# Kernel tuning notes

Hardware: AMD Instinct MI355X
Metric: run time of the kernel (lower is better)

Reference implementation:

```python
import jax, jax.numpy as jnp
import numpy as np

B = 1_000_000
NG = 4          # distance_embed_dim -> 4x0e scalars per edge feature
MAX_OFF = 5.0   # max_cross_offset (GaussianSmearing stop)

# e3nn FullyConnectedTensorProduct path coefficients:
#   coeff = sqrt(dim(ir_out) / fan_in_elements) * w3j_entry
# where w3j entries are 1 (000), 1/sqrt(3) (011/101/110), eps/sqrt(6) (111).
# tp1: irreps (4x0e+1e) x (4x0e+1e) -> 20x0e + 5x1e
#   fan_in(0e) = 4*4 + 1*1 = 17 ; fan_in(1e) = 4*1 + 1*4 + 1*1 = 9
C1_000 = (1.0 / 17.0) ** 0.5
C1_110 = (1.0 / 17.0) ** 0.5 / 3.0 ** 0.5
C1_011 = (3.0 / 9.0) ** 0.5 / 3.0 ** 0.5
C1_101 = C1_011
C1_111 = (3.0 / 9.0) ** 0.5 / 6.0 ** 0.5
# tp2: (20x0e+5x1e) x (4x0e+1e) -> 9x0e + 1x1e
#   fan_in(0e) = 20*4 + 5*1 = 85 ; fan_in(1e) = 20*1 + 5*4 + 5*1 = 45
C2_000 = (1.0 / 85.0) ** 0.5
C2_110 = (1.0 / 85.0) ** 0.5 / 3.0 ** 0.5
C2_011 = (3.0 / 45.0) ** 0.5 / 3.0 ** 0.5
C2_101 = C2_011
C2_111 = (3.0 / 45.0) ** 0.5 / 6.0 ** 0.5


def setup_inputs() -> dict:
    key = jax.random.key(0)
    ks = jax.random.split(key, 12)
    f32 = jnp.float32
    return dict(
        ligand=jax.random.normal(ks[0], (B, 4, 3), f32),
        receptor=jax.random.normal(ks[1], (B, 4, 3), f32) + 1.0,
        # tp1 weights (mul-1 axes squeezed): paths 000,110,011,101,111
        w1_000=jax.random.normal(ks[2], (NG, NG, 20), f32),
        w1_110=jax.random.normal(ks[3], (20,), f32),
        w1_011=jax.random.normal(ks[4], (NG, 5), f32),
        w1_101=jax.random.normal(ks[5], (NG, 5), f32),
        w1_111=jax.random.normal(ks[6], (5,), f32),
        # tp2 weights
        w2_000=jax.random.normal(ks[7], (20, NG, 9), f32),
        w2_110=jax.random.normal(ks[8], (5, 9), f32),
        w2_011=jax.random.normal(ks[9], (20,), f32),
        w2_101=jax.random.normal(ks[10], (5, NG), f32),
        w2_111=jax.random.normal(ks[11], (5,), f32),
    )


def _forward(ligand, receptor, w1_000, w1_110, w1_011, w1_101, w1_111,
             w2_000, w2_110, w2_011, w2_101, w2_111):
    edge_vec = ligand - receptor                                 # (B,4,3)
    dist = jnp.sqrt(jnp.sum(edge_vec * edge_vec, -1, keepdims=True))  # (B,4,1)
    offset = jnp.linspace(0.0, MAX_OFF, NG).astype(ligand.dtype)  # (NG,)
    coeff = -0.5 / (offset[1] - offset[0]) ** 2
    emb = jnp.exp(coeff * (dist - offset) ** 2)                  # (B,4,NG)
    unit = edge_vec / dist                                       # (B,4,3)
    s1, v1 = emb[:, 1], unit[:, 1]
    s2, v2 = emb[:, 2], unit[:, 2]
    s3, v3 = emb[:, 3], unit[:, 3]
    # ---- tp1: (s1,v1) x (s2,v2) -> S (B,20), V (B,5,3) ----
    dot12 = jnp.sum(v1 * v2, -1)                                 # (B,)
    S = (C1_000 * jnp.einsum('uvw,bu,bv->bw', w1_000, s1, s2)
         + C1_110 * dot12[:, None] * w1_110)
    cr12 = jnp.cross(v1, v2)                                     # (B,3)
    V = (C1_011 * jnp.einsum('uw,bu,bk->bwk', w1_011, s1, v2)
         + C1_101 * jnp.einsum('vw,bv,bk->bwk', w1_101, s2, v1)
         + C1_111 * w1_111[None, :, None] * cr12[:, None, :])
    # ---- tp2: (S,V) x (s3,v3) -> out (B,12) = 9x0e + 1x1e ----
    Vd3 = jnp.einsum('buk,bk->bu', V, v3)                        # (B,5)
    S2 = (C2_000 * jnp.einsum('uvw,bu,bv->bw', w2_000, S, s3)
          + C2_110 * jnp.einsum('uw,bu->bw', w2_110, Vd3))
    Vx3 = jnp.cross(V, v3[:, None, :])                           # (B,5,3)
    V2 = (C2_011 * jnp.einsum('u,bu,bk->bk', w2_011, S, v3)
          + C2_101 * jnp.einsum('uv,buk,bv->bk', w2_101, V, s3)
          + C2_111 * jnp.einsum('u,buk->bk', w2_111, Vx3))
    return jnp.concatenate([S2, V2], -1)                         # (B,12)


def reference(ligand, receptor, w1_000, w1_110, w1_011, w1_101, w1_111,
              w2_000, w2_110, w2_011, w2_101, w2_111):
    out = _forward(ligand, receptor, w1_000, w1_110, w1_011, w1_101, w1_111,
                   w2_000, w2_110, w2_011, w2_101, w2_111)
    s_rot, s_tr = out[:, :3], out[:, 3:6]
    t_rot, t_tr = out[:, 6:9], out[:, 9:12]
    return s_rot, s_tr, t_rot, t_tr
```

## Files before the change

kernel.cpp:

```cpp
#include <hip/hip_runtime.h>
#include <math.h>


#define K_A   (0.10846522890932808f * 0.24253562503633297f)
#define K_B   (0.10846522890932808f * 0.14002800840979312f)
#define K_P   (0.06262242910851495f * 0.33333333333333333f)
#define K_Q   (0.06262242910851495f * 0.33333333333333333f)
#define K_R   (0.06262242910851495f * 0.23570226039551584f)
#define K_WB  (0.14907119849998599f * 0.24253562503633297f)
#define K_CB  (0.14907119849998599f * 0.14002800840979312f)
#define K_WA  (0.14907119849998599f * 0.33333333333333333f)
#define K_WBT (0.14907119849998599f * 0.33333333333333333f)
#define K_WC  (0.14907119849998599f * 0.23570226039551584f)
#define K_WA3 (0.10540925533894598f * 0.33333333333333333f)
#define K_WB3 (0.10540925533894598f * 0.33333333333333333f)
#define K_WC3 (0.10540925533894598f * 0.23570226039551584f)

#define EX_WB   720
#define EX_CB   736
#define EX_WA   740
#define EX_WBT  756
#define EX_WC   772
#define EX_WA3  776
#define EX_WB3  780
#define EX_WC3  784
#define N_WS    785

__global__ void fd8_prep(const float* __restrict__ w1_000, const float* __restrict__ w1_110,
                         const float* __restrict__ w1_011, const float* __restrict__ w1_101,
                         const float* __restrict__ w1_111, const float* __restrict__ w2_000,
                         const float* __restrict__ w2_110, const float* __restrict__ w2_011,
                         const float* __restrict__ w2_101, const float* __restrict__ w2_111,
                         float* __restrict__ ws)
{
    int j = threadIdx.x;
    if (j >= N_WS) return;
    float val = 0.f;
    if (j < 720) {
        int r = j / 9, c = j - r * 9;
        if (r < 64) {
            int pq = r >> 2, v = r & 3;
            float a = 0.f;
            for (int u = 0; u < 20; ++u)
                a = fmaf(w1_000[pq * 20 + u], w2_000[u * 36 + v * 9 + c], a);
            val = K_A * a;
        } else if (r < 68) {
            int v = r - 64; float a = 0.f;
            for (int u = 0; u < 20; ++u)
                a = fmaf(w1_110[u], w2_000[u * 36 + v * 9 + c], a);
            val = K_B * a;
        } else if (r < 72) {
            int u = r - 68; float a = 0.f;
            for (int m = 0; m < 5; ++m)
                a = fmaf(w1_011[u * 5 + m], w2_110[m * 9 + c], a);
            val = K_P * a;
        } else if (r < 76) {
            int u = r - 72; float a = 0.f;
            for (int m = 0; m < 5; ++m)
                a = fmaf(w1_101[u * 5 + m], w2_110[m * 9 + c], a);
            val = K_Q * a;
        } else if (r == 76) {
            float a = 0.f;
            for (int m = 0; m < 5; ++m)
                a = fmaf(w1_111[m], w2_110[m * 9 + c], a);
            val = K_R * a;
        }
    } else {
        int k = j - 720;
        if (k < 16) {
            float a = 0.f;
            for (int u = 0; u < 20; ++u)
                a = fmaf(w2_011[u], w1_000[k * 20 + u], a);
            val = K_WB * a;
        } else if (k == 16) {
            float a = 0.f;
            for (int u = 0; u < 20; ++u)
                a = fmaf(w2_011[u], w1_110[u], a);
            val = K_CB * a;
        } else if (k >= 20 && k < 36) {
            int u = (k - 20) >> 2, v = (k - 20) & 3;
            float a = 0.f;
            for (int m = 0; m < 5; ++m)
                a = fmaf(w1_011[u * 5 + m], w2_101[m * 4 + v], a);
            val = K_WA * a;
        } else if (k >= 36 && k < 52) {
            int u = (k - 36) >> 2, v = (k - 36) & 3;
            float a = 0.f;
            for (int m = 0; m < 5; ++m)
                a = fmaf(w1_101[u * 5 + m], w2_101[m * 4 + v], a);
            val = K_WBT * a;
        } else if (k >= 52 && k < 56) {
            int v = k - 52; float a = 0.f;
            for (int m = 0; m < 5; ++m)
                a = fmaf(w1_111[m], w2_101[m * 4 + v], a);
            val = K_WC * a;
        } else if (k >= 56 && k < 60) {
            int u = k - 56; float a = 0.f;
            for (int m = 0; m < 5; ++m)
                a = fmaf(w2_111[m], w1_011[u * 5 + m], a);
            val = K_WA3 * a;
        } else if (k >= 60 && k < 64) {
            int v = k - 60; float a = 0.f;
            for (int m = 0; m < 5; ++m)
                a = fmaf(w2_111[m], w1_101[v * 5 + m], a);
            val = K_WB3 * a;
        } else if (k == 64) {
            float a = 0.f;
            for (int m = 0; m < 5; ++m)
                a = fmaf(w2_111[m], w1_111[m], a);
            val = K_WC3 * a;
        }
    }
    ws[j] = val;
}

__global__ __launch_bounds__(256) void
fd8(const float* __restrict__ lig, const float* __restrict__ rec,
    const float* __restrict__ ws, float* __restrict__ out, int n)
{
    const int tid = blockIdx.x * 256 + threadIdx.x;
    if (tid >= n) return;

    const float4* L = (const float4*)(lig + (size_t)tid * 12);
    const float4* R = (const float4*)(rec + (size_t)tid * 12);
    float4 l0 = L[0], l1 = L[1], l2 = L[2];
    float4 r0 = R[0], r1 = R[1], r2 = R[2];

    float e1x = l0.w - r0.w, e1y = l1.x - r1.x, e1z = l1.y - r1.y;
    float e2x = l1.z - r1.z, e2y = l1.w - r1.w, e2z = l2.x - r2.x;
    float e3x = l2.y - r2.y, e3y = l2.z - r2.z, e3z = l2.w - r2.w;

    float n1 = fmaf(e1x, e1x, fmaf(e1y, e1y, e1z * e1z));
    float n2 = fmaf(e2x, e2x, fmaf(e2y, e2y, e2z * e2z));
    float n3sq = fmaf(e3x, e3x, fmaf(e3y, e3y, e3z * e3z));
    float i1 = __builtin_amdgcn_rsqf(n1);
    float i2 = __builtin_amdgcn_rsqf(n2);
    float i3 = __builtin_amdgcn_rsqf(n3sq);
    float d1 = n1 * i1, d2 = n2 * i2, d3 = n3sq * i3;

    float v1x = e1x * i1, v1y = e1y * i1, v1z = e1z * i1;
    float v2x = e2x * i2, v2y = e2y * i2, v2z = e2z * i2;
    float v3x = e3x * i3, v3y = e3y * i3, v3z = e3z * i3;

    const float coeff = -0.18f;
    const float o1 = 1.6666666f, o2 = 3.3333333f, o3 = 5.f;
    float s1[4], s2[4], s3[4];
    float x;
    x = d1;      s1[0] = __expf(coeff * x * x);
    x = d1 - o1; s1[1] = __expf(coeff * x * x);
    x = d1 - o2; s1[2] = __expf(coeff * x * x);
    x = d1 - o3; s1[3] = __expf(coeff * x * x);
    x = d2;      s2[0] = __expf(coeff * x * x);
    x = d2 - o1; s2[1] = __expf(coeff * x * x);
    x = d2 - o2; s2[2] = __expf(coeff * x * x);
    x = d2 - o3; s2[3] = __expf(coeff * x * x);
    x = d3;      s3[0] = __expf(coeff * x * x);
    x = d3 - o1; s3[1] = __expf(coeff * x * x);
    x = d3 - o2; s3[2] = __expf(coeff * x * x);
    x = d3 - o3; s3[3] = __expf(coeff * x * x);

    float dot12 = v1x * v2x + v1y * v2y + v1z * v2z;
    float d13   = v1x * v3x + v1y * v3y + v1z * v3z;
    float d23   = v2x * v3x + v2y * v3y + v2z * v3z;
    float c12x = v1y * v2z - v1z * v2y;
    float c12y = v1z * v2x - v1x * v2z;
    float c12z = v1x * v2y - v1y * v2x;
    float dtp  = c12x * v3x + c12y * v3y + c12z * v3z;

    float acc0 = 0.f, acc1 = 0.f, acc2 = 0.f, acc3 = 0.f, acc4 = 0.f;
    float acc5 = 0.f, acc6 = 0.f, acc7 = 0.f, acc8 = 0.f;

#define GROUP4(g, x0v, x1v, x2v, x3v) do { \
    const float* wp_ = ws + 36 * (g); \
    const float x0_ = (x0v), x1_ = (x1v), x2_ = (x2v), x3_ = (x3v); \
    acc0 = fmaf(x0_, wp_[0], acc0);  acc1 = fmaf(x0_, wp_[1], acc1); \
    acc2 = fmaf(x0_, wp_[2], acc2);  acc3 = fmaf(x0_, wp_[3], acc3); \
    acc4 = fmaf(x0_, wp_[4], acc4);  acc5 = fmaf(x0_, wp_[5], acc5); \
    acc6 = fmaf(x0_, wp_[6], acc6);  acc7 = fmaf(x0_, wp_[7], acc7); \
    acc8 = fmaf(x0_, wp_[8], acc8); \
    acc0 = fmaf(x1_, wp_[9], acc0);  acc1 = fmaf(x1_, wp_[10], acc1); \
    acc2 = fmaf(x1_, wp_[11], acc2); acc3 = fmaf(x1_, wp_[12], acc3); \
    acc4 = fmaf(x1_, wp_[13], acc4); acc5 = fmaf(x1_, wp_[14], acc5); \
    acc6 = fmaf(x1_, wp_[15], acc6); acc7 = fmaf(x1_, wp_[16], acc7); \
    acc8 = fmaf(x1_, wp_[17], acc8); \
    acc0 = fmaf(x2_, wp_[18], acc0); acc1 = fmaf(x2_, wp_[19], acc1); \
    acc2 = fmaf(x2_, wp_[20], acc2); acc3 = fmaf(x2_, wp_[21], acc3); \
    acc4 = fmaf(x2_, wp_[22], acc4); acc5 = fmaf(x2_, wp_[23], acc5); \
    acc6 = fmaf(x2_, wp_[24], acc6); acc7 = fmaf(x2_, wp_[25], acc7); \
    acc8 = fmaf(x2_, wp_[26], acc8); \
    acc0 = fmaf(x3_, wp_[27], acc0); acc1 = fmaf(x3_, wp_[28], acc1); \
    acc2 = fmaf(x3_, wp_[29], acc2); acc3 = fmaf(x3_, wp_[30], acc3); \
    acc4 = fmaf(x3_, wp_[31], acc4); acc5 = fmaf(x3_, wp_[32], acc5); \
    acc6 = fmaf(x3_, wp_[33], acc6); acc7 = fmaf(x3_, wp_[34], acc7); \
    acc8 = fmaf(x3_, wp_[35], acc8); \
} while (0)

    float sg = dot12 * ws[EX_CB];

#pragma unroll
    for (int p = 0; p < 4; ++p) {
#pragma unroll
        for (int q = 0; q < 4; ++q) {
            const int pq = p * 4 + q;
            float o = s1[p] * s2[q];
            sg = fmaf(o, ws[EX_WB + pq], sg);
            GROUP4(pq, o * s3[0], o * s3[1], o * s3[2], o * s3[3]);
        }
    }
    GROUP4(16, dot12 * s3[0], dot12 * s3[1], dot12 * s3[2], dot12 * s3[3]);
    GROUP4(17, d23 * s1[0], d23 * s1[1], d23 * s1[2], d23 * s1[3]);
    GROUP4(18, d13 * s2[0], d13 * s2[1], d13 * s2[2], d13 * s2[3]);
    {
        const float* wp = ws + 36 * 19;
        acc0 = fmaf(dtp, wp[0], acc0); acc1 = fmaf(dtp, wp[1], acc1);
        acc2 = fmaf(dtp, wp[2], acc2); acc3 = fmaf(dtp, wp[3], acc3);
        acc4 = fmaf(dtp, wp[4], acc4); acc5 = fmaf(dtp, wp[5], acc5);
        acc6 = fmaf(dtp, wp[6], acc6); acc7 = fmaf(dtp, wp[7], acc7);
        acc8 = fmaf(dtp, wp[8], acc8);
    }
#undef GROUP4

    float ta = 0.f, tb = 0.f;
#pragma unroll
    for (int u = 0; u < 4; ++u) {
        float da = fmaf(ws[EX_WA + u * 4 + 0], s3[0], fmaf(ws[EX_WA + u * 4 + 1], s3[1],
                   fmaf(ws[EX_WA + u * 4 + 2], s3[2], ws[EX_WA + u * 4 + 3] * s3[3])));
        float db = fmaf(ws[EX_WBT + u * 4 + 0], s3[0], fmaf(ws[EX_WBT + u * 4 + 1], s3[1],
                   fmaf(ws[EX_WBT + u * 4 + 2], s3[2], ws[EX_WBT + u * 4 + 3] * s3[3])));
        ta = fmaf(s1[u], da, ta);
        tb = fmaf(s2[u], db, tb);
    }
    float tc = fmaf(ws[EX_WC + 0], s3[0], fmaf(ws[EX_WC + 1], s3[1],
               fmaf(ws[EX_WC + 2], s3[2], ws[EX_WC + 3] * s3[3])));
    float wa = fmaf(ws[EX_WA3 + 0], s1[0], fmaf(ws[EX_WA3 + 1], s1[1],
               fmaf(ws[EX_WA3 + 2], s1[2], ws[EX_WA3 + 3] * s1[3])));
    float wb = fmaf(ws[EX_WB3 + 0], s2[0], fmaf(ws[EX_WB3 + 1], s2[1],
               fmaf(ws[EX_WB3 + 2], s2[2], ws[EX_WB3 + 3] * s2[3])));
    float wc = ws[EX_WC3];

    float c23x = v2y * v3z - v2z * v3y;
    float c23y = v2z * v3x - v2x * v3z;
    float c23z = v2x * v3y - v2y * v3x;
    float c13x = v1y * v3z - v1z * v3y;
    float c13y = v1z * v3x - v1x * v3z;
    float c13z = v1x * v3y - v1y * v3x;
    float ccrx = c12y * v3z - c12z * v3y;
    float ccry = c12z * v3x - c12x * v3z;
    float ccrz = c12x * v3y - c12y * v3x;

    float V2x = sg * v3x + ta * v2x + tb * v1x + tc * c12x + wa * c23x + wb * c13x + wc * ccrx;
    float V2y = sg * v3y + ta * v2y + tb * v1y + tc * c12y + wa * c23y + wb * c13y + wc * ccry;
    float V2z = sg * v3z + ta * v2z + tb * v1z + tc * c12z + wa * c23z + wb * c13z + wc * ccrz;

    const size_t n3 = (size_t)n * 3;
    const size_t base = (size_t)tid * 3;
    out[base + 0] = acc0;
    out[base + 1] = acc1;
    out[base + 2] = acc2;
    out[n3 + base + 0] = acc3;
    out[n3 + base + 1] = acc4;
    out[n3 + base + 2] = acc5;
    out[2 * n3 + base + 0] = acc6;
    out[2 * n3 + base + 1] = acc7;
    out[2 * n3 + base + 2] = acc8;
    out[3 * n3 + base + 0] = V2x;
    out[3 * n3 + base + 1] = V2y;
    out[3 * n3 + base + 2] = V2z;
}

extern "C" void kernel_launch(void* const* d_in, const int* in_sizes, int n_in,
                              void* d_out, int out_size, void* d_ws, size_t ws_size,
                              hipStream_t stream) {
    const float* lig = (const float*)d_in[0];
    const float* rec = (const float*)d_in[1];
    float* ws = (float*)d_ws;

    fd8_prep<<<1, 1024, 0, stream>>>(
        (const float*)d_in[2], (const float*)d_in[3], (const float*)d_in[4],
        (const float*)d_in[5], (const float*)d_in[6], (const float*)d_in[7],
        (const float*)d_in[8], (const float*)d_in[9], (const float*)d_in[10],
        (const float*)d_in[11], ws);

    int n = in_sizes[0] / 12;
    int blocks = (n + 255) / 256;
    fd8<<<blocks, 256, 0, stream>>>(lig, rec, ws, (float*)d_out, n);
}
```

Baseline: 162.6 us.

## Process two items per thread with packed FP32 FMAs and paired stores

Each thread now handles two batch items, computing geometry for both and then accumulating the 9 scalar outputs with two-wide vector FMAs (v2f) over a reordered weight layout, so one weight load pair serves two packed lanes. The prep kernel permutes the fused weight table into interleaved column pairs to match, and runs on four blocks. Output writes become float2 stores covering both items. The aim is to use packed FP32 math and halve the scalar weight loads per item, at the cost of more registers per thread and possibly lower occupancy.

```diff
diff --git a/kernel.cpp b/kernel.cpp
--- a/kernel.cpp
+++ b/kernel.cpp
@@ -26,40 +26,46 @@
 #define EX_WC3  784
 #define N_WS    785
 
-__global__ void fd8_prep(const float* __restrict__ w1_000, const float* __restrict__ w1_110,
-                         const float* __restrict__ w1_011, const float* __restrict__ w1_101,
-                         const float* __restrict__ w1_111, const float* __restrict__ w2_000,
-                         const float* __restrict__ w2_110, const float* __restrict__ w2_011,
-                         const float* __restrict__ w2_101, const float* __restrict__ w2_111,
-                         float* __restrict__ ws)
+typedef float v2f __attribute__((ext_vector_type(2)));
+
+__global__ void fd10_prep(const float* __restrict__ w1_000, const float* __restrict__ w1_110,
+                          const float* __restrict__ w1_011, const float* __restrict__ w1_101,
+                          const float* __restrict__ w1_111, const float* __restrict__ w2_000,
+                          const float* __restrict__ w2_110, const float* __restrict__ w2_011,
+                          const float* __restrict__ w2_101, const float* __restrict__ w2_111,
+                          float* __restrict__ ws)
 {
-    int j = threadIdx.x;
+    int j = blockIdx.x * 256 + threadIdx.x;
     if (j >= N_WS) return;
     float val = 0.f;
     if (j < 720) {
-        int r = j / 9, c = j - r * 9;
-        if (r < 64) {
-            int pq = r >> 2, v = r & 3;
+        int g = j / 36, slot = j - g * 36;
+        int r, c;
+        if (slot < 32) { r = (slot & 7) >> 1; c = ((slot >> 3) << 1) + (slot & 1); }
+        else           { r = slot - 32;       c = 8; }
+        int R = 4 * g + r;
+        if (R < 64) {
+            int pq = R >> 2, v = R & 3;
             float a = 0.f;
             for (int u = 0; u < 20; ++u)
                 a = fmaf(w1_000[pq * 20 + u], w2_000[u * 36 + v * 9 + c], a);
             val = K_A * a;
-        } else if (r < 68) {
-            int v = r - 64; float a = 0.f;
+        } else if (R < 68) {
+            int v = R - 64; float a = 0.f;
             for (int u = 0; u < 20; ++u)
                 a = fmaf(w1_110[u], w2_000[u * 36 + v * 9 + c], a);
             val = K_B * a;
-        } else if (r < 72) {
-            int u = r - 68; float a = 0.f;
+        } else if (R < 72) {
+            int u = R - 68; float a = 0.f;
             for (int m = 0; m < 5; ++m)
                 a = fmaf(w1_011[u * 5 + m], w2_110[m * 9 + c], a);
             val = K_P * a;
-        } else if (r < 76) {
-            int u = r - 72; float a = 0.f;
+        } else if (R < 76) {
+            int u = R - 72; float a = 0.f;
             for (int m = 0; m < 5; ++m)
                 a = fmaf(w1_101[u * 5 + m], w2_110[m * 9 + c], a);
             val = K_Q * a;
-        } else if (r == 76) {
+        } else if (R == 76) {
             float a = 0.f;
             for (int m = 0; m < 5; ++m)
                 a = fmaf(w1_111[m], w2_110[m * 9 + c], a);
@@ -114,158 +120,205 @@
     ws[j] = val;
 }
 
-__global__ __launch_bounds__(256) void
-fd8(const float* __restrict__ lig, const float* __restrict__ rec,
-    const float* __restrict__ ws, float* __restrict__ out, int n)
+struct ItemState {
+    float s1[4], s2[4], s3[4];
+    float dot12, d13, d23, dtp;
+    float v3x, v3y, v3z;
+    float px, py, pz;
+};
+
+__device__ __forceinline__ ItemState geom(const float4 l0, const float4 l1, const float4 l2,
+                                          const float4 r0, const float4 r1, const float4 r2,
+                                          const float* __restrict__ ws)
 {
-    const int tid = blockIdx.x * 256 + threadIdx.x;
-    if (tid >= n) return;
-
-    const float4* L = (const float4*)(lig + (size_t)tid * 12);
-    const float4* R = (const float4*)(rec + (size_t)tid * 12);
-    float4 l0 = L[0], l1 = L[1], l2 = L[2];
-    float4 r0 = R[0], r1 = R[1], r2 = R[2];
-
+    ItemState st;
     float e1x = l0.w - r0.w, e1y = l1.x - r1.x, e1z = l1.y - r1.y;
     float e2x = l1.z - r1.z, e2y = l1.w - r1.w, e2z = l2.x - r2.x;
     float e3x = l2.y - r2.y, e3y = l2.z - r2.z, e3z = l2.w - r2.w;
 
     float n1 = fmaf(e1x, e1x, fmaf(e1y, e1y, e1z * e1z));
     float n2 = fmaf(e2x, e2x, fmaf(e2y, e2y, e2z * e2z));
-    float n3sq = fmaf(e3x, e3x, fmaf(e3y, e3y, e3z * e3z));
+    float n3q = fmaf(e3x, e3x, fmaf(e3y, e3y, e3z * e3z));
     float i1 = __builtin_amdgcn_rsqf(n1);
     float i2 = __builtin_amdgcn_rsqf(n2);
-    float i3 = __builtin_amdgcn_rsqf(n3sq);
-    float d1 = n1 * i1, d2 = n2 * i2, d3 = n3sq * i3;
+    float i3 = __builtin_amdgcn_rsqf(n3q);
+    float d1 = n1 * i1, d2 = n2 * i2, d3 = n3q * i3;
 
     float v1x = e1x * i1, v1y = e1y * i1, v1z = e1z * i1;
     float v2x = e2x * i2, v2y = e2y * i2, v2z = e2z * i2;
-    float v3x = e3x * i3, v3y = e3y * i3, v3z = e3z * i3;
+    st.v3x = e3x * i3; st.v3y = e3y * i3; st.v3z = e3z * i3;
 
     const float coeff = -0.18f;
     const float o1 = 1.6666666f, o2 = 3.3333333f, o3 = 5.f;
-    float s1[4], s2[4], s3[4];
     float x;
-    x = d1;      s1[0] = __expf(coeff * x * x);
-    x = d1 - o1; s1[1] = __expf(coeff * x * x);
-    x = d1 - o2; s1[2] = __expf(coeff * x * x);
-    x = d1 - o3; s1[3] = __expf(coeff * x * x);
-    x = d2;      s2[0] = __expf(coeff * x * x);
-    x = d2 - o1; s2[1] = __expf(coeff * x * x);
-    x = d2 - o2; s2[2] = __expf(coeff * x * x);
-    x = d2 - o3; s2[3] = __expf(coeff * x * x);
-    x = d3;      s3[0] = __expf(coeff * x * x);
-    x = d3 - o1; s3[1] = __expf(coeff * x * x);
-    x = d3 - o2; s3[2] = __expf(coeff * x * x);
-    x = d3 - o3; s3[3] = __expf(coeff * x * x);
-
-    float dot12 = v1x * v2x + v1y * v2y + v1z * v2z;
-    float d13   = v1x * v3x + v1y * v3y + v1z * v3z;
-    float d23   = v2x * v3x + v2y * v3y + v2z * v3z;
+    x = d1;      st.s1[0] = __expf(coeff * x * x);
+    x = d1 - o1; st.s1[1] = __expf(coeff * x * x);
+    x = d1 - o2; st.s1[2] = __expf(coeff * x * x);
+    x = d1 - o3; st.s1[3] = __expf(coeff * x * x);
+    x = d2;      st.s2[0] = __expf(coeff * x * x);
+    x = d2 - o1; st.s2[1] = __expf(coeff * x * x);
+    x = d2 - o2; st.s2[2] = __expf(coeff * x * x);
+    x = d2 - o3; st.s2[3] = __expf(coeff * x * x);
+    x = d3;      st.s3[0] = __expf(coeff * x * x);
+    x = d3 - o1; st.s3[1] = __expf(coeff * x * x);
+    x = d3 - o2; st.s3[2] = __expf(coeff * x * x);
+    x = d3 - o3; st.s3[3] = __expf(coeff * x * x);
+
+    st.dot12 = v1x * v2x + v1y * v2y + v1z * v2z;
+    st.d13   = v1x * st.v3x + v1y * st.v3y + v1z * st.v3z;
+    st.d23   = v2x * st.v3x + v2y * st.v3y + v2z * st.v3z;
     float c12x = v1y * v2z - v1z * v2y;
     float c12y = v1z * v2x - v1x * v2z;
     float c12z = v1x * v2y - v1y * v2x;
-    float dtp  = c12x * v3x + c12y * v3y + c12z * v3z;
-
-    float acc0 = 0.f, acc1 = 0.f, acc2 = 0.f, acc3 = 0.f, acc4 = 0.f;
-    float acc5 = 0.f, acc6 = 0.f, acc7 = 0.f, acc8 = 0.f;
-
-#define GROUP4(g, x0v, x1v, x2v, x3v) do { \
+    st.dtp = c12x * st.v3x + c12y * st.v3y + c12z * st.v3z;
+
+    float ta = 0.f, tb = 0.f;
+#pragma unroll
+    for (int u = 0; u < 4; ++u) {
+        float da = fmaf(ws[EX_WA + u * 4 + 0], st.s3[0], fmaf(ws[EX_WA + u * 4 + 1], st.s3[1],
+                   fmaf(ws[EX_WA + u * 4 + 2], st.s3[2], ws[EX_WA + u * 4 + 3] * st.s3[3])));
+        float db = fmaf(ws[EX_WBT + u * 4 + 0], st.s3[0], fmaf(ws[EX_WBT + u * 4 + 1], st.s3[1],
+                   fmaf(ws[EX_WBT + u * 4 + 2], st.s3[2], ws[EX_WBT + u * 4 + 3] * st.s3[3])));
+        ta = fmaf(st.s1[u], da, ta);
+        tb = fmaf(st.s2[u], db, tb);
+    }
+    float tc = fmaf(ws[EX_WC + 0], st.s3[0], fmaf(ws[EX_WC + 1], st.s3[1],
+               fmaf(ws[EX_WC + 2], st.s3[2], ws[EX_WC + 3] * st.s3[3])));
+    float wa = fmaf(ws[EX_WA3 + 0], st.s1[0], fmaf(ws[EX_WA3 + 1], st.s1[1],
+               fmaf(ws[EX_WA3 + 2], st.s1[2], ws[EX_WA3 + 3] * st.s1[3])));
+    float wb = fmaf(ws[EX_WB3 + 0], st.s2[0], fmaf(ws[EX_WB3 + 1], st.s2[1],
+               fmaf(ws[EX_WB3 + 2], st.s2[2], ws[EX_WB3 + 3] * st.s2[3])));
+    float wc = ws[EX_WC3];
+
+    float c23x = v2y * st.v3z - v2z * st.v3y;
+    float c23y = v2z * st.v3x - v2x * st.v3z;
+    float c23z = v2x * st.v3y - v2y * st.v3x;
+    float c13x = v1y * st.v3z - v1z * st.v3y;
+    float c13y = v1z * st.v3x - v1x * st.v3z;
+    float c13z = v1x * st.v3y - v1y * st.v3x;
+    float ccrx = c12y * st.v3z - c12z * st.v3y;
+    float ccry = c12z * st.v3x - c12x * st.v3z;
+    float ccrz = c12x * st.v3y - c12y * st.v3x;
+
+    st.px = ta * v2x + tb * v1x + tc * c12x + wa * c23x + wb * c13x + wc * ccrx;
+    st.py = ta * v2y + tb * v1y + tc * c12y + wa * c23y + wb * c13y + wc * ccry;
+    st.pz = ta * v2z + tb * v1z + tc * c12z + wa * c23z + wb * c13z + wc * ccrz;
+    return st;
+}
+
+__global__ __launch_bounds__(256) void
+fd10(const float* __restrict__ lig, const float* __restrict__ rec,
+     const float* __restrict__ ws, float* __restrict__ out, int n)
+{
+    const int t = blockIdx.x * 256 + threadIdx.x;
+    const size_t iA = (size_t)t * 2;
+    if (iA >= (size_t)n) return;
+    const bool two = (iA + 1) < (size_t)n;
+    const size_t iB = two ? iA + 1 : iA;
+
+    const float4* LA = (const float4*)(lig + iA * 12);
+    const float4* RA = (const float4*)(rec + iA * 12);
+    const float4* LB = (const float4*)(lig + iB * 12);
+    const float4* RB = (const float4*)(rec + iB * 12);
+    float4 lA0 = LA[0], lA1 = LA[1], lA2 = LA[2];
+    float4 rA0 = RA[0], rA1 = RA[1], rA2 = RA[2];
+    float4 lB0 = LB[0], lB1 = LB[1], lB2 = LB[2];
+    float4 rB0 = RB[0], rB1 = RB[1], rB2 = RB[2];
+
+    ItemState A = geom(lA0, lA1, lA2, rA0, rA1, rA2, ws);
+    __builtin_amdgcn_sched_barrier(0);
+    ItemState B = geom(lB0, lB1, lB2, rB0, rB1, rB2, ws);
+    __builtin_amdgcn_sched_barrier(0);
+
+    v2f a01A = {0.f, 0.f}, a23A = {0.f, 0.f}, a45A = {0.f, 0.f}, a67A = {0.f, 0.f};
+    v2f a01B = {0.f, 0.f}, a23B = {0.f, 0.f}, a45B = {0.f, 0.f}, a67B = {0.f, 0.f};
+    float a8A = 0.f, a8B = 0.f;
+
+#define FMA2(x_, wptr_, accv_) accv_ = __builtin_elementwise_fma((v2f){(x_), (x_)}, *(const v2f*)(wptr_), accv_)
+
+#define GROUP4D(g, xa0, xa1, xa2, xa3, xb0, xb1, xb2, xb3) do { \
     const float* wp_ = ws + 36 * (g); \
-    const float x0_ = (x0v), x1_ = (x1v), x2_ = (x2v), x3_ = (x3v); \
-    acc0 = fmaf(x0_, wp_[0], acc0);  acc1 = fmaf(x0_, wp_[1], acc1); \
-    acc2 = fmaf(x0_, wp_[2], acc2);  acc3 = fmaf(x0_, wp_[3], acc3); \
-    acc4 = fmaf(x0_, wp_[4], acc4);  acc5 = fmaf(x0_, wp_[5], acc5); \
-    acc6 = fmaf(x0_, wp_[6], acc6);  acc7 = fmaf(x0_, wp_[7], acc7); \
-    acc8 = fmaf(x0_, wp_[8], acc8); \
-    acc0 = fmaf(x1_, wp_[9], acc0);  acc1 = fmaf(x1_, wp_[10], acc1); \
-    acc2 = fmaf(x1_, wp_[11], acc2); acc3 = fmaf(x1_, wp_[12], acc3); \
-    acc4 = fmaf(x1_, wp_[13], acc4); acc5 = fmaf(x1_, wp_[14], acc5); \
-    acc6 = fmaf(x1_, wp_[15], acc6); acc7 = fmaf(x1_, wp_[16], acc7); \
-    acc8 = fmaf(x1_, wp_[17], acc8); \
-    acc0 = fmaf(x2_, wp_[18], acc0); acc1 = fmaf(x2_, wp_[19], acc1); \
-    acc2 = fmaf(x2_, wp_[20], acc2); acc3 = fmaf(x2_, wp_[21], acc3); \
-    acc4 = fmaf(x2_, wp_[22], acc4); acc5 = fmaf(x2_, wp_[23], acc5); \
-    acc6 = fmaf(x2_, wp_[24], acc6); acc7 = fmaf(x2_, wp_[25], acc7); \
-    acc8 = fmaf(x2_, wp_[26], acc8); \
-    acc0 = fmaf(x3_, wp_[27], acc0); acc1 = fmaf(x3_, wp_[28], acc1); \
-    acc2 = fmaf(x3_, wp_[29], acc2); acc3 = fmaf(x3_, wp_[30], acc3); \
-    acc4 = fmaf(x3_, wp_[31], acc4); acc5 = fmaf(x3_, wp_[32], acc5); \
-    acc6 = fmaf(x3_, wp_[33], acc6); acc7 = fmaf(x3_, wp_[34], acc7); \
-    acc8 = fmaf(x3_, wp_[35], acc8); \
+    const float a0_ = (xa0), a1_ = (xa1), a2_ = (xa2), a3_ = (xa3); \
+    const float b0_ = (xb0), b1_ = (xb1), b2_ = (xb2), b3_ = (xb3); \
+    FMA2(a0_, wp_ +  0, a01A); FMA2(a0_, wp_ +  8, a23A); FMA2(a0_, wp_ + 16, a45A); FMA2(a0_, wp_ + 24, a67A); a8A = fmaf(a0_, wp_[32], a8A); \
+    FMA2(b0_, wp_ +  0, a01B); FMA2(b0_, wp_ +  8, a23B); FMA2(b0_, wp_ + 16, a45B); FMA2(b0_, wp_ + 24, a67B); a8B = fmaf(b0_, wp_[32], a8B); \
+    FMA2(a1_, wp_ +  2, a01A); FMA2(a1_, wp_ + 10, a23A); FMA2(a1_, wp_ + 18, a45A); FMA2(a1_, wp_ + 26, a67A); a8A = fmaf(a1_, wp_[33], a8A); \
+    FMA2(b1_, wp_ +  2, a01B); FMA2(b1_, wp_ + 10, a23B); FMA2(b1_, wp_ + 18, a45B); FMA2(b1_, wp_ + 26, a67B); a8B = fmaf(b1_, wp_[33], a8B); \
+    FMA2(a2_, wp_ +  4, a01A); FMA2(a2_, wp_ + 12, a23A); FMA2(a2_, wp_ + 20, a45A); FMA2(a2_, wp_ + 28, a67A); a8A = fmaf(a2_, wp_[34], a8A); \
+    FMA2(b2_, wp_ +  4, a01B); FMA2(b2_, wp_ + 12, a23B); FMA2(b2_, wp_ + 20, a45B); FMA2(b2_, wp_ + 28, a67B); a8B = fmaf(b2_, wp_[34], a8B); \
+    FMA2(a3_, wp_ +  6, a01A); FMA2(a3_, wp_ + 14, a23A); FMA2(a3_, wp_ + 22, a45A); FMA2(a3_, wp_ + 30, a67A); a8A = fmaf(a3_, wp_[35], a8A); \
+    FMA2(b3_, wp_ +  6, a01B); FMA2(b3_, wp_ + 14, a23B); FMA2(b3_, wp_ + 22, a45B); FMA2(b3_, wp_ + 30, a67B); a8B = fmaf(b3_, wp_[35], a8B); \
 } while (0)
 
-    float sg = dot12 * ws[EX_CB];
+    const float cb = ws[EX_CB];
+    float sgA = A.dot12 * cb, sgB = B.dot12 * cb;
 
 #pragma unroll
     for (int p = 0; p < 4; ++p) {
 #pragma unroll
         for (int q = 0; q < 4; ++q) {
             const int pq = p * 4 + q;
-            float o = s1[p] * s2[q];
-            sg = fmaf(o, ws[EX_WB + pq], sg);
-            GROUP4(pq, o * s3[0], o * s3[1], o * s3[2], o * s3[3]);
+            const float oA = A.s1[p] * A.s2[q];
+            const float oB = B.s1[p] * B.s2[q];
+            const float wbq = ws[EX_WB + pq];
+            sgA = fmaf(oA, wbq, sgA);
+            sgB = fmaf(oB, wbq, sgB);
+            GROUP4D(pq, oA * A.s3[0], oA * A.s3[1], oA * A.s3[2], oA * A.s3[3],
+                        oB * B.s3[0], oB * B.s3[1], oB * B.s3[2], oB * B.s3[3]);
         }
     }
-    GROUP4(16, dot12 * s3[0], dot12 * s3[1], dot12 * s3[2], dot12 * s3[3]);
-    GROUP4(17, d23 * s1[0], d23 * s1[1], d23 * s1[2], d23 * s1[3]);
-    GROUP4(18, d13 * s2[0], d13 * s2[1], d13 * s2[2], d13 * s2[3]);
+    GROUP4D(16, A.dot12 * A.s3[0], A.dot12 * A.s3[1], A.dot12 * A.s3[2], A.dot12 * A.s3[3],
+                B.dot12 * B.s3[0], B.dot12 * B.s3[1], B.dot12 * B.s3[2], B.dot12 * B.s3[3]);
+    GROUP4D(17, A.d23 * A.s1[0], A.d23 * A.s1[1], A.d23 * A.s1[2], A.d23 * A.s1[3],
+                B.d23 * B.s1[0], B.d23 * B.s1[1], B.d23 * B.s1[2], B.d23 * B.s1[3]);
+    GROUP4D(18, A.d13 * A.s2[0], A.d13 * A.s2[1], A.d13 * A.s2[2], A.d13 * A.s2[3],
+                B.d13 * B.s2[0], B.d13 * B.s2[1], B.d13 * B.s2[2], B.d13 * B.s2[3]);
     {
         const float* wp = ws + 36 * 19;
-        acc0 = fmaf(dtp, wp[0], acc0); acc1 = fmaf(dtp, wp[1], acc1);
-        acc2 = fmaf(dtp, wp[2], acc2); acc3 = fmaf(dtp, wp[3], acc3);
-        acc4 = fmaf(dtp, wp[4], acc4); acc5 = fmaf(dtp, wp[5], acc5);
-        acc6 = fmaf(dtp, wp[6], acc6); acc7 = fmaf(dtp, wp[7], acc7);
-        acc8 = fmaf(dtp, wp[8], acc8);
-    }
-#undef GROUP4
-
-    float ta = 0.f, tb = 0.f;
-#pragma unroll
-    for (int u = 0; u < 4; ++u) {
-        float da = fmaf(ws[EX_WA + u * 4 + 0], s3[0], fmaf(ws[EX_WA + u * 4 + 1], s3[1],
-                   fmaf(ws[EX_WA + u * 4 + 2], s3[2], ws[EX_WA + u * 4 + 3] * s3[3])));
-        float db = fmaf(ws[EX_WBT + u * 4 + 0], s3[0], fmaf(ws[EX_WBT + u * 4 + 1], s3[1],
-                   fmaf(ws[EX_WBT + u * 4 + 2], s3[2], ws[EX_WBT + u * 4 + 3] * s3[3])));
-        ta = fmaf(s1[u], da, ta);
-        tb = fmaf(s2[u], db, tb);
-    }
-    float tc = fmaf(ws[EX_WC + 0], s3[0], fmaf(ws[EX_WC + 1], s3[1],
-               fmaf(ws[EX_WC + 2], s3[2], ws[EX_WC + 3] * s3[3])));
-    float wa = fmaf(ws[EX_WA3 + 0], s1[0], fmaf(ws[EX_WA3 + 1], s1[1],
-               fmaf(ws[EX_WA3 + 2], s1[2], ws[EX_WA3 + 3] * s1[3])));
-    float wb = fmaf(ws[EX_WB3 + 0], s2[0], fmaf(ws[EX_WB3 + 1], s2[1],
-               fmaf(ws[EX_WB3 + 2], s2[2], ws[EX_WB3 + 3] * s2[3])));
-    float wc = ws[EX_WC3];
-
-    float c23x = v2y * v3z - v2z * v3y;
-    float c23y = v2z * v3x - v2x * v3z;
-    float c23z = v2x * v3y - v2y * v3x;
-    float c13x = v1y * v3z - v1z * v3y;
-    float c13y = v1z * v3x - v1x * v3z;
-    float c13z = v1x * v3y - v1y * v3x;
-    float ccrx = c12y * v3z - c12z * v3y;
-    float ccry = c12z * v3x - c12x * v3z;
-    float ccrz = c12x * v3y - c12y * v3x;
-
-    float V2x = sg * v3x + ta * v2x + tb * v1x + tc * c12x + wa * c23x + wb * c13x + wc * ccrx;
-    float V2y = sg * v3y + ta * v2y + tb * v1y + tc * c12y + wa * c23y + wb * c13y + wc * ccry;
-    float V2z = sg * v3z + ta * v2z + tb * v1z + tc * c12z + wa * c23z + wb * c13z + wc * ccrz;
+        FMA2(A.dtp, wp +  0, a01A); FMA2(A.dtp, wp +  8, a23A);
+        FMA2(A.dtp, wp + 16, a45A); FMA2(A.dtp, wp + 24, a67A); a8A = fmaf(A.dtp, wp[32], a8A);
+        FMA2(B.dtp, wp +  0, a01B); FMA2(B.dtp, wp +  8, a23B);
+        FMA2(B.dtp, wp + 16, a45B); FMA2(B.dtp, wp + 24, a67B); a8B = fmaf(B.dtp, wp[32], a8B);
+    }
+#undef GROUP4D
+#undef FMA2
+
+    float V2xA = fmaf(sgA, A.v3x, A.px);
+    float V2yA = fmaf(sgA, A.v3y, A.py);
+    float V2zA = fmaf(sgA, A.v3z, A.pz);
+    float V2xB = fmaf(sgB, B.v3x, B.px);
+    float V2yB = fmaf(sgB, B.v3y, B.py);
+    float V2zB = fmaf(sgB, B.v3z, B.pz);
 
     const size_t n3 = (size_t)n * 3;
-    const size_t base = (size_t)tid * 3;
-    out[base + 0] = acc0;
-    out[base + 1] = acc1;
-    out[base + 2] = acc2;
-    out[n3 + base + 0] = acc3;
-    out[n3 + base + 1] = acc4;
-    out[n3 + base + 2] = acc5;
-    out[2 * n3 + base + 0] = acc6;
-    out[2 * n3 + base + 1] = acc7;
-    out[2 * n3 + base + 2] = acc8;
-    out[3 * n3 + base + 0] = V2x;
-    out[3 * n3 + base + 1] = V2y;
-    out[3 * n3 + base + 2] = V2z;
+    const size_t base = iA * 3;
+    if (two) {
+        *(float2*)(out + base + 0)          = make_float2(a01A[0], a01A[1]);
+        *(float2*)(out + base + 2)          = make_float2(a23A[0], a01B[0]);
+        *(float2*)(out + base + 4)          = make_float2(a01B[1], a23B[0]);
+        *(float2*)(out + n3 + base + 0)     = make_float2(a23A[1], a45A[0]);
+        *(float2*)(out + n3 + base + 2)     = make_float2(a45A[1], a23B[1]);
+        *(float2*)(out + n3 + base + 4)     = make_float2(a45B[0], a45B[1]);
+        *(float2*)(out + 2 * n3 + base + 0) = make_float2(a67A[0], a67A[1]);
+        *(float2*)(out + 2 * n3 + base + 2) = make_float2(a8A, a67B[0]);
+        *(float2*)(out + 2 * n3 + base + 4) = make_float2(a67B[1], a8B);
+        *(float2*)(out + 3 * n3 + base + 0) = make_float2(V2xA, V2yA);
+        *(float2*)(out + 3 * n3 + base + 2) = make_float2(V2zA, V2xB);
+        *(float2*)(out + 3 * n3 + base + 4) = make_float2(V2yB, V2zB);
+    } else {
+        out[base + 0] = a01A[0];
+        out[base + 1] = a01A[1];
+        out[base + 2] = a23A[0];
+        out[n3 + base + 0] = a23A[1];
+        out[n3 + base + 1] = a45A[0];
+        out[n3 + base + 2] = a45A[1];
+        out[2 * n3 + base + 0] = a67A[0];
+        out[2 * n3 + base + 1] = a67A[1];
+        out[2 * n3 + base + 2] = a8A;
+        out[3 * n3 + base + 0] = V2xA;
+        out[3 * n3 + base + 1] = V2yA;
+        out[3 * n3 + base + 2] = V2zA;
+    }
 }
 
 extern "C" void kernel_launch(void* const* d_in, const int* in_sizes, int n_in,
@@ -275,13 +328,14 @@
     const float* rec = (const float*)d_in[1];
     float* ws = (float*)d_ws;
 
-    fd8_prep<<<1, 1024, 0, stream>>>(
+    fd10_prep<<<4, 256, 0, stream>>>(
         (const float*)d_in[2], (const float*)d_in[3], (const float*)d_in[4],
         (const float*)d_in[5], (const float*)d_in[6], (const float*)d_in[7],
         (const float*)d_in[8], (const float*)d_in[9], (const float*)d_in[10],
         (const float*)d_in[11], ws);
 
     int n = in_sizes[0] / 12;
-    int blocks = (n + 255) / 256;
-    fd8<<<blocks, 256, 0, stream>>>(lig, rec, ws, (float*)d_out, n);
+    int nPairs = (n + 1) / 2;
+    int blocks = (nPairs + 255) / 256;
+    fd10<<<blocks, 256, 0, stream>>>(lig, rec, ws, (float*)d_out, n);
 }
```

Result: slower. 186.4 us (+14.6%).
